# Kernel optimization log

Measured on AMD Instinct MI355X. Metric: run time of the kernel, lower is better.

## Reference

```python
import jax, jax.numpy as jnp
import numpy as np
import math

B, S, E = 2, 2048, 1024
H, HD = 16, 64  # num_heads, head_size


def setup_inputs() -> dict:
    key = jax.random.key(0)
    ks = jax.random.split(key, 9)
    sc = 1.0 / math.sqrt(HD)
    return {
        "x": jax.random.normal(ks[0], (B, S, E), dtype=jnp.float32),
        "Wq_w": jax.random.normal(ks[1], (HD, HD), dtype=jnp.float32) * sc,
        "Wq_b": jax.random.normal(ks[2], (HD,), dtype=jnp.float32) * 0.02,
        "Wk_w": jax.random.normal(ks[3], (HD, HD), dtype=jnp.float32) * sc,
        "Wk_b": jax.random.normal(ks[4], (HD,), dtype=jnp.float32) * 0.02,
        "Wv_w": jax.random.normal(ks[5], (HD, HD), dtype=jnp.float32) * sc,
        "Wv_b": jax.random.normal(ks[6], (HD,), dtype=jnp.float32) * 0.02,
        "proj_w": jax.random.normal(ks[7], (E, E), dtype=jnp.float32) * (1.0 / math.sqrt(E)),
        "proj_b": jax.random.normal(ks[8], (E,), dtype=jnp.float32) * 0.02,
    }


def reference(x, Wq_w, Wq_b, Wk_w, Wk_b, Wv_w, Wv_b, proj_w, proj_b):
    b, s, _ = x.shape
    xh = x.reshape(b, s, H, HD)  # split heads; QKV linears act per-head (shared weights)
    # torch Linear: y = x @ W.T + b
    q = jnp.einsum('bshd,ed->bhse', xh, Wq_w) + Wq_b  # [B,H,S,HD]
    k = jnp.einsum('bshd,ed->bhse', xh, Wk_w) + Wk_b
    v = jnp.einsum('bshd,ed->bhse', xh, Wv_w) + Wv_b
    scores = jnp.einsum('bhqd,bhkd->bhqk', q, k) / math.sqrt(HD)
    causal = jnp.tril(jnp.ones((s, s), dtype=bool))
    scores = jnp.where(causal, scores, jnp.float32(-1e20))
    attn = jax.nn.softmax(scores, axis=-1)  # attn_dropout p=0 (eval)
    out = jnp.einsum('bhqk,bhkd->bqhd', attn, v).reshape(b, s, H * HD)
    out = out @ proj_w.T + proj_b  # resid_dropout p=0 (eval)
    return out
```

## Files before the change

kernel.cpp:

```cpp
#include <hip/hip_runtime.h>
#include <hip/hip_bf16.h>

#define B_ 2
#define S_ 2048
#define E_ 1024
#define H_ 16
#define HD_ 64
#define T_ (B_ * S_)

typedef short bf16x8 __attribute__((ext_vector_type(8)));
typedef short bf16x4 __attribute__((ext_vector_type(4)));
typedef float f32x4 __attribute__((ext_vector_type(4)));

__device__ __forceinline__ short f2bf(float f) {
  union { float f; unsigned u; } v;
  v.f = f;
  unsigned r = v.u + 0x7fffu + ((v.u >> 16) & 1u);
  return (short)(r >> 16);
}

__device__ __forceinline__ int vperm_key(int cc) {
  return (cc & ~31) | (((cc >> 2) & 1) << 4) | (((cc >> 3) & 3) << 2) | (cc & 3);
}

__global__ __launch_bounds__(256) void qkv_conv_kernel(
    const float* __restrict__ x,
    const float* __restrict__ wq, const float* __restrict__ bq,
    const float* __restrict__ wk, const float* __restrict__ bk,
    const float* __restrict__ wv, const float* __restrict__ bv,
    short* __restrict__ Q, short* __restrict__ K, short* __restrict__ V,
    const float* __restrict__ pw, short* __restrict__ pwb) {
  const int tid = threadIdx.x;
  if (blockIdx.x >= 512) {
    int i = ((blockIdx.x - 512) * 256 + tid) * 4;
    float4 f = *(const float4*)(pw + i);
    bf16x4 o;
    o[0] = f2bf(f.x); o[1] = f2bf(f.y); o[2] = f2bf(f.z); o[3] = f2bf(f.w);
    *(bf16x4*)(pwb + i) = o;
    return;
  }
  __shared__ short Xs[64][136];
  __shared__ short Ws[192][72];
  __shared__ short Qt[64][68], Kt[64][68], Vt[64][68];

  const int bid = blockIdx.x;
  const int tb = bid >> 3, hg = bid & 7;
  const int s0 = (tb * 64) & (S_ - 1);
  const int bb = (tb * 64) >> 11;
  const int wave = tid >> 6, lane = tid & 63;
  const int lrow = lane & 15, quad = lane >> 4;

#pragma unroll
  for (int i = 0; i < 8; i++) {
    int c = tid + 256 * i;
    int row = c >> 5, col4 = c & 31;
    float4 f = *(const float4*)(x + ((long)(tb * 64 + row)) * E_ + hg * 128 + col4 * 4);
    bf16x4 o;
    o[0] = f2bf(f.x); o[1] = f2bf(f.y); o[2] = f2bf(f.z); o[3] = f2bf(f.w);
    *(bf16x4*)&Xs[row][col4 * 4] = o;
  }
#pragma unroll
  for (int m = 0; m < 3; m++) {
    const float* w = (m == 0) ? wq : (m == 1) ? wk : wv;
#pragma unroll
    for (int i = 0; i < 4; i++) {
      int c = tid + 256 * i;
      int row = m * 64 + (c >> 4), col = (c & 15) * 4;
      float4 f = *(const float4*)(w + (long)c * 4);
      bf16x4 o;
      o[0] = f2bf(f.x); o[1] = f2bf(f.y); o[2] = f2bf(f.z); o[3] = f2bf(f.w);
      *(bf16x4*)&Ws[row][col] = o;
    }
  }
  float bias[12];
#pragma unroll
  for (int nb = 0; nb < 12; nb++) {
    int sel = nb >> 2;
    int e = ((nb & 3) * 16) + lrow;
    bias[nb] = ((sel == 0) ? bq : (sel == 1) ? bk : bv)[e];
  }
  __syncthreads();

  bf16x8 bf0[12], bf1[12];
#pragma unroll
  for (int nb = 0; nb < 12; nb++) {
    bf0[nb] = *(bf16x8*)&Ws[nb * 16 + lrow][quad * 8];
    bf1[nb] = *(bf16x8*)&Ws[nb * 16 + lrow][32 + quad * 8];
  }

  const float QSCALE = 0.125f * 1.44269504089f;
  for (int hl = 0; hl < 2; hl++) {
    const int h = hg * 2 + hl;
    bf16x8 a0 = *(bf16x8*)&Xs[wave * 16 + lrow][hl * 64 + quad * 8];
    bf16x8 a1 = *(bf16x8*)&Xs[wave * 16 + lrow][hl * 64 + 32 + quad * 8];
#pragma unroll
    for (int nb = 0; nb < 12; nb++) {
      f32x4 acc = {0.f, 0.f, 0.f, 0.f};
      acc = __builtin_amdgcn_mfma_f32_16x16x32_bf16(a0, bf0[nb], acc, 0, 0, 0);
      acc = __builtin_amdgcn_mfma_f32_16x16x32_bf16(a1, bf1[nb], acc, 0, 0, 0);
      const int sel = nb >> 2;
      const float scale = (sel == 0) ? QSCALE : 1.0f;
      short (*ct)[68] = (sel == 0) ? Qt : (sel == 1) ? Kt : Vt;
#pragma unroll
      for (int r = 0; r < 4; r++) {
        ct[wave * 16 + quad * 4 + r][(nb & 3) * 16 + lrow] =
            f2bf((acc[r] + bias[nb]) * scale);
      }
    }
    __syncthreads();

    const int bh = bb * H_ + h;
    short* Qg = Q + ((long)bh * S_ + s0) * HD_;
    short* Kg = K + ((long)bh * S_ + s0) * HD_;
    short* Vg = V + (long)bh * HD_ * S_;
#pragma unroll
    for (int i = 0; i < 2; i++) {
      int c = tid + 256 * i;
      int row = c >> 3, col = (c & 7) * 8;
      *(bf16x8*)(Qg + (long)row * HD_ + col) = *(bf16x8*)&Qt[row][col];
      *(bf16x8*)(Kg + (long)row * HD_ + col) = *(bf16x8*)&Kt[row][col];
      bf16x8 vv;
#pragma unroll
      for (int j = 0; j < 8; j++) {
        int cc = col + j;
        vv[j] = Vt[vperm_key(cc)][row];
      }
      *(bf16x8*)(Vg + (long)row * S_ + s0 + col) = vv;
    }
    __syncthreads();
  }
}

__global__ __launch_bounds__(256, 4) void attn_kernel(
    const short* __restrict__ Q, const short* __restrict__ K,
    const short* __restrict__ Vt, short* __restrict__ O ) {
  __shared__ __align__(16) char RAW[2 * 64 * 72 * 2 * 2];
  short (*Ks)[64][72] = (short (*)[64][72])RAW;
  short (*Vs)[64][72] = (short (*)[64][72])(RAW + 2 * 64 * 72 * 2);
  float (*Cb)[64][20] = (float (*)[64][20])RAW;

  const int tid = threadIdx.x;
  const int bid = blockIdx.x;
  const int bh = bid & 31;
  const int pr = bid >> 5;
  const int b = bh >> 4, h = bh & 15;
  const long base = ((long)bh) << 17;

  const int wave = tid >> 6, lane = tid & 63;
  const int c = wave >> 1;
  const int s = wave & 1;
  const int lrow = lane & 15, quad = lane >> 4;

  const int ct = tid & 127;
  const int r0 = ct >> 1, chc = (ct & 1) * 32;
  const short* Kg = K + base + (long)r0 * HD_ + chc;
  const short* Vg = Vt + base + (long)r0 * S_ + chc;

  bf16x8 kreg[4], vreg[4];
  auto LD = [&](int k0) {
#pragma unroll
    for (int j = 0; j < 4; j++) {
      kreg[j] = *(const bf16x8*)(Kg + (long)k0 * HD_ + 8 * j);
      vreg[j] = *(const bf16x8*)(Vg + k0 + 8 * j);
    }
  };

  const int qts[2] = {pr, 63 - pr};
  LD(c * 64);
  bool nextld = false;

  for (int ph = 0; ph < 2; ph++) {
    const int qt = qts[ph];
    const int nkt = (qt >> 1) + 1;
    const int nc = (nkt + 1 - c) >> 1;
    const int nit = (nkt + 1) >> 1;
    if (ph == 1 && !nextld) LD(c * 64);

    const int qg = qt * 32 + s * 16 + lrow;
    const short* qp = Q + base + (long)qg * HD_;
    bf16x8 qf0 = *(const bf16x8*)(qp + quad * 8);
    bf16x8 qf1 = *(const bf16x8*)(qp + 32 + quad * 8);

    f32x4 Oacc[4];
#pragma unroll
    for (int db = 0; db < 4; db++) Oacc[db] = f32x4{0.f, 0.f, 0.f, 0.f};
    float lsum = 0.f;

    for (int i = 0; i < nit; i++) {
      const bool act = i < nc;
      const int kt = 2 * i + c;
      if (act) {
#pragma unroll
        for (int j = 0; j < 4; j++) {
          *(bf16x8*)&Ks[c][r0][chc + 8 * j] = kreg[j];
          *(bf16x8*)&Vs[c][r0][chc + 8 * j] = vreg[j];
        }
      }
      __syncthreads();
      if (i + 1 < nc) {
        LD((2 * (i + 1) + c) * 64);
      } else if (ph == 0 && i + 1 == nc) {
        LD(c * 64);
        nextld = true;
      }

      if (act) {
        f32x4 sc[4];
#pragma unroll
        for (int nb = 0; nb < 4; nb++) {
          bf16x8 ka0 = *(bf16x8*)&Ks[c][nb * 16 + lrow][quad * 8];
          bf16x8 ka1 = *(bf16x8*)&Ks[c][nb * 16 + lrow][32 + quad * 8];
          f32x4 acc = {0.f, 0.f, 0.f, 0.f};
          acc = __builtin_amdgcn_mfma_f32_16x16x32_bf16(ka0, qf0, acc, 0, 0, 0);
          acc = __builtin_amdgcn_mfma_f32_16x16x32_bf16(ka1, qf1, acc, 0, 0, 0);
          sc[nb] = acc;
        }

        if (kt == nkt - 1) {
          const int k0 = kt * 64;
#pragma unroll
          for (int nb = 0; nb < 4; nb++) {
            int kgl = k0 + nb * 16 + quad * 4;
#pragma unroll
            for (int r = 0; r < 4; r++)
              if (kgl + r > qg) sc[nb][r] = -1e30f;
          }
        }

        bf16x4 pf[4];
#pragma unroll
        for (int nb = 0; nb < 4; nb++) {
          unsigned u[4];
#pragma unroll
          for (int r = 0; r < 4; r++) {
            float p = __builtin_amdgcn_exp2f(sc[nb][r]);
            lsum += p;
            u[r] = __float_as_uint(p) + 0x8000u;
          }
          unsigned lo = __builtin_amdgcn_perm(u[1], u[0], 0x07060302u);
          unsigned hi = __builtin_amdgcn_perm(u[3], u[2], 0x07060302u);
          union { unsigned q[2]; bf16x4 v; } pk;
          pk.q[0] = lo; pk.q[1] = hi;
          pf[nb] = pk.v;
        }

#pragma unroll
        for (int p2 = 0; p2 < 2; p2++) {
#pragma unroll
          for (int db = 0; db < 4; db++) {
            bf16x8 vv = *(bf16x8*)&Vs[c][db * 16 + lrow][p2 * 32 + quad * 8];
            bf16x4 vlo = {vv[0], vv[1], vv[2], vv[3]};
            bf16x4 vhi = {vv[4], vv[5], vv[6], vv[7]};
            Oacc[db] = __builtin_amdgcn_mfma_f32_16x16x16bf16_1k(vlo, pf[2 * p2], Oacc[db], 0, 0, 0);
            Oacc[db] = __builtin_amdgcn_mfma_f32_16x16x16bf16_1k(vhi, pf[2 * p2 + 1], Oacc[db], 0, 0, 0);
          }
        }
      }
      __syncthreads();
    }

    if (c == 1) {
#pragma unroll
      for (int db = 0; db < 4; db++) {
        float4 o4 = make_float4(Oacc[db][0], Oacc[db][1], Oacc[db][2], Oacc[db][3]);
        *(float4*)&Cb[s][lane][db * 4] = o4;
      }
      Cb[s][lane][16] = lsum;
    }
    __syncthreads();
    if (c == 0) {
#pragma unroll
      for (int db = 0; db < 4; db++) {
        float4 o4 = *(float4*)&Cb[s][lane][db * 4];
        Oacc[db][0] += o4.x; Oacc[db][1] += o4.y;
        Oacc[db][2] += o4.z; Oacc[db][3] += o4.w;
      }
      lsum += Cb[s][lane][16];
      lsum += __shfl_xor(lsum, 16);
      lsum += __shfl_xor(lsum, 32);
      const float invl = 1.f / lsum;
      const long token = (long)b * S_ + qg;
      short* obase = O + token * E_ + h * HD_;
#pragma unroll
      for (int db = 0; db < 4; db++) {
        bf16x4 o;
#pragma unroll
        for (int r = 0; r < 4; r++) o[r] = f2bf(Oacc[db][r] * invl);
        *(bf16x4*)(obase + db * 16 + quad * 4) = o;
      }
    }
    __syncthreads();
  }
}

__global__ __launch_bounds__(256) void proj_kernel(
    const short* __restrict__ A, const short* __restrict__ W,
    const float* __restrict__ bias, float* __restrict__ out) {
  __shared__ short As[2][128][40];
  __shared__ short Bs[2][64][40];
  const int tid = threadIdx.x;
  const int bid = blockIdx.x;
  const int m0 = (bid >> 4) * 128;
  const int n0 = (bid & 15) * 64;
  const int wave = tid >> 6, lane = tid & 63;
  const int wm = wave >> 1, wn = wave & 1;
  const int lrow = lane & 15, quad = lane >> 4;

  const int ar = tid >> 1, ac = (tid & 1) * 16;
  const int br = tid >> 2, bc = (tid & 3) * 8;

  bf16x8 a0, a1, b0;
  auto LDR = [&](int k0) {
    const short* ap = A + (long)(m0 + ar) * E_ + k0 + ac;
    a0 = *(const bf16x8*)(ap);
    a1 = *(const bf16x8*)(ap + 8);
    b0 = *(const bf16x8*)(W + (long)(n0 + br) * E_ + k0 + bc);
  };

  f32x4 acc[4][2];
#pragma unroll
  for (int i = 0; i < 4; i++)
#pragma unroll
    for (int j = 0; j < 2; j++) acc[i][j] = f32x4{0.f, 0.f, 0.f, 0.f};

  LDR(0);
  for (int kk = 0; kk < 32; kk++) {
    const int buf = kk & 1;
    *(bf16x8*)&As[buf][ar][ac] = a0;
    *(bf16x8*)&As[buf][ar][ac + 8] = a1;
    *(bf16x8*)&Bs[buf][br][bc] = b0;
    __syncthreads();
    if (kk < 31) LDR((kk + 1) * 32);

    bf16x8 af[4], bfr[2];
#pragma unroll
    for (int i = 0; i < 4; i++)
      af[i] = *(bf16x8*)&As[buf][wm * 64 + i * 16 + lrow][quad * 8];
#pragma unroll
    for (int j = 0; j < 2; j++)
      bfr[j] = *(bf16x8*)&Bs[buf][wn * 32 + j * 16 + lrow][quad * 8];
#pragma unroll
    for (int i = 0; i < 4; i++)
#pragma unroll
      for (int j = 0; j < 2; j++)
        acc[i][j] = __builtin_amdgcn_mfma_f32_16x16x32_bf16(af[i], bfr[j], acc[i][j], 0, 0, 0);
  }

#pragma unroll
  for (int j = 0; j < 2; j++) {
    int col = n0 + wn * 32 + j * 16 + lrow;
    float bv = bias[col];
#pragma unroll
    for (int i = 0; i < 4; i++) {
#pragma unroll
      for (int r = 0; r < 4; r++) {
        int row = m0 + wm * 64 + i * 16 + quad * 4 + r;
        out[(long)row * E_ + col] = acc[i][j][r] + bv;
      }
    }
  }
}

extern "C" void kernel_launch(void* const* d_in, const int* in_sizes, int n_in,
                              void* d_out, int out_size, void* d_ws, size_t ws_size,
                              hipStream_t stream) {
  const float* x  = (const float*)d_in[0];
  const float* wq = (const float*)d_in[1];
  const float* bq = (const float*)d_in[2];
  const float* wk = (const float*)d_in[3];
  const float* bk = (const float*)d_in[4];
  const float* wv = (const float*)d_in[5];
  const float* bv = (const float*)d_in[6];
  const float* pw = (const float*)d_in[7];
  const float* pb = (const float*)d_in[8];
  float* out = (float*)d_out;

  char* ws = (char*)d_ws;
  const size_t qkv_bytes = (size_t)B_ * H_ * S_ * HD_ * 2;
  short* Qb = (short*)(ws);
  short* Kb = (short*)(ws + qkv_bytes);
  short* Vb = (short*)(ws + 2 * qkv_bytes);
  short* AO = (short*)(ws + 3 * qkv_bytes);
  short* PW = (short*)(ws + 3 * qkv_bytes + (size_t)T_ * E_ * 2);

  qkv_conv_kernel<<<dim3(512 + 1024), dim3(256), 0, stream>>>(
      x, wq, bq, wk, bk, wv, bv, Qb, Kb, Vb, pw, PW);
  attn_kernel<<<dim3(32 * 32), dim3(256), 0, stream>>>(Qb, Kb, Vb, AO);
  proj_kernel<<<dim3(32 * 16), dim3(256), 0, stream>>>(AO, PW, pb, out);
}
```

Baseline: 157.8 us.

## Pre-swizzle K/V tiles into MFMA fragment order and restructure attention blocking

```diff
diff --git a/kernel.cpp b/kernel.cpp
--- a/kernel.cpp
+++ b/kernel.cpp
@@ -19,16 +19,13 @@
   return (short)(r >> 16);
 }
 
-__device__ __forceinline__ int vperm_key(int cc) {
-  return (cc & ~31) | (((cc >> 2) & 1) << 4) | (((cc >> 3) & 3) << 2) | (cc & 3);
-}
 
 __global__ __launch_bounds__(256) void qkv_conv_kernel(
     const float* __restrict__ x,
     const float* __restrict__ wq, const float* __restrict__ bq,
     const float* __restrict__ wk, const float* __restrict__ bk,
     const float* __restrict__ wv, const float* __restrict__ bv,
-    short* __restrict__ Q, short* __restrict__ K, short* __restrict__ V,
+    short* __restrict__ Q, short* __restrict__ KV,
     const float* __restrict__ pw, short* __restrict__ pwb) {
   const int tid = threadIdx.x;
   if (blockIdx.x >= 512) {
@@ -46,6 +43,7 @@
   const int bid = blockIdx.x;
   const int tb = bid >> 3, hg = bid & 7;
   const int s0 = (tb * 64) & (S_ - 1);
+  const int kt = s0 >> 6;
   const int bb = (tb * 64) >> 11;
   const int wave = tid >> 6, lane = tid & 63;
   const int lrow = lane & 15, quad = lane >> 4;
@@ -111,73 +109,70 @@
 
     const int bh = bb * H_ + h;
     short* Qg = Q + ((long)bh * S_ + s0) * HD_;
-    short* Kg = K + ((long)bh * S_ + s0) * HD_;
-    short* Vg = V + (long)bh * HD_ * S_;
+    short* Tg = KV + ((long)(bh * 32 + kt)) * 8192;
 #pragma unroll
     for (int i = 0; i < 2; i++) {
       int c = tid + 256 * i;
       int row = c >> 3, col = (c & 7) * 8;
       *(bf16x8*)(Qg + (long)row * HD_ + col) = *(bf16x8*)&Qt[row][col];
-      *(bf16x8*)(Kg + (long)row * HD_ + col) = *(bf16x8*)&Kt[row][col];
-      bf16x8 vv;
-#pragma unroll
-      for (int j = 0; j < 8; j++) {
-        int cc = col + j;
-        vv[j] = Vt[vperm_key(cc)][row];
-      }
-      *(bf16x8*)(Vg + (long)row * S_ + s0 + col) = vv;
+    }
+#pragma unroll
+    for (int u = 0; u < 4; u++) {
+      int fid = tid + 256 * u;
+      bf16x8 val;
+      int lane2 = fid & 63;
+      int quad2 = lane2 >> 4, lrow2 = lane2 & 15;
+      if (u < 2) {
+        int g = fid >> 6;
+        int nb = g >> 1, half = g & 1;
+        val = *(bf16x8*)&Kt[nb * 16 + lrow2][half * 32 + quad2 * 8];
+      } else {
+        int g = (fid >> 6) & 7;
+        int p2 = g >> 2, db = g & 3;
+#pragma unroll
+        for (int j = 0; j < 8; j++) {
+          int key = (2 * p2 + (j >> 2)) * 16 + quad2 * 4 + (j & 3);
+          val[j] = Vt[key][db * 16 + lrow2];
+        }
+      }
+      *(bf16x8*)(Tg + fid * 8) = val;
     }
     __syncthreads();
   }
 }
 
-__global__ __launch_bounds__(256, 4) void attn_kernel(
-    const short* __restrict__ Q, const short* __restrict__ K,
-    const short* __restrict__ Vt, short* __restrict__ O ) {
-  __shared__ __align__(16) char RAW[2 * 64 * 72 * 2 * 2];
-  short (*Ks)[64][72] = (short (*)[64][72])RAW;
-  short (*Vs)[64][72] = (short (*)[64][72])(RAW + 2 * 64 * 72 * 2);
-  float (*Cb)[64][20] = (float (*)[64][20])RAW;
+__global__ __launch_bounds__(256) void attn_kernel(
+    const short* __restrict__ Q, const short* __restrict__ KV,
+    short* __restrict__ O ) {
+  __shared__ short L[2][8192];
 
   const int tid = threadIdx.x;
   const int bid = blockIdx.x;
   const int bh = bid & 31;
   const int pr = bid >> 5;
   const int b = bh >> 4, h = bh & 15;
-  const long base = ((long)bh) << 17;
+  const long qbase = ((long)bh) << 17;
 
   const int wave = tid >> 6, lane = tid & 63;
-  const int c = wave >> 1;
-  const int s = wave & 1;
   const int lrow = lane & 15, quad = lane >> 4;
 
-  const int ct = tid & 127;
-  const int r0 = ct >> 1, chc = (ct & 1) * 32;
-  const short* Kg = K + base + (long)r0 * HD_ + chc;
-  const short* Vg = Vt + base + (long)r0 * S_ + chc;
-
-  bf16x8 kreg[4], vreg[4];
-  auto LD = [&](int k0) {
-#pragma unroll
-    for (int j = 0; j < 4; j++) {
-      kreg[j] = *(const bf16x8*)(Kg + (long)k0 * HD_ + 8 * j);
-      vreg[j] = *(const bf16x8*)(Vg + k0 + 8 * j);
-    }
+  const short* Tg = KV + ((long)bh * 32) * 8192 + tid * 8;
+
+  bf16x8 reg[4];
+  auto LD = [&](int kt) {
+    const short* p = Tg + (long)kt * 8192;
+#pragma unroll
+    for (int u = 0; u < 4; u++) reg[u] = *(const bf16x8*)(p + u * 2048);
   };
 
-  const int qts[2] = {pr, 63 - pr};
-  LD(c * 64);
-  bool nextld = false;
-
+  const int qts[2] = {pr, 31 - pr};
+  LD(0);
+  int it = 0;
   for (int ph = 0; ph < 2; ph++) {
     const int qt = qts[ph];
-    const int nkt = (qt >> 1) + 1;
-    const int nc = (nkt + 1 - c) >> 1;
-    const int nit = (nkt + 1) >> 1;
-    if (ph == 1 && !nextld) LD(c * 64);
-
-    const int qg = qt * 32 + s * 16 + lrow;
-    const short* qp = Q + base + (long)qg * HD_;
+    const int q0w = qt * 64 + wave * 16;
+    const int qg = q0w + lrow;
+    const short* qp = Q + qbase + (long)qg * HD_;
     bf16x8 qf0 = *(const bf16x8*)(qp + quad * 8);
     bf16x8 qf1 = *(const bf16x8*)(qp + 32 + quad * 8);
 
@@ -186,110 +181,87 @@
     for (int db = 0; db < 4; db++) Oacc[db] = f32x4{0.f, 0.f, 0.f, 0.f};
     float lsum = 0.f;
 
-    for (int i = 0; i < nit; i++) {
-      const bool act = i < nc;
-      const int kt = 2 * i + c;
-      if (act) {
-#pragma unroll
-        for (int j = 0; j < 4; j++) {
-          *(bf16x8*)&Ks[c][r0][chc + 8 * j] = kreg[j];
-          *(bf16x8*)&Vs[c][r0][chc + 8 * j] = vreg[j];
-        }
-      }
+    const int nkt = qt + 1;
+    for (int kt = 0; kt < nkt; kt++, it++) {
+      const int buf = it & 1;
+#pragma unroll
+      for (int u = 0; u < 4; u++)
+        *(bf16x8*)&L[buf][(tid + 256 * u) * 8] = reg[u];
       __syncthreads();
-      if (i + 1 < nc) {
-        LD((2 * (i + 1) + c) * 64);
-      } else if (ph == 0 && i + 1 == nc) {
-        LD(c * 64);
-        nextld = true;
-      }
-
-      if (act) {
-        f32x4 sc[4];
+
+      {
+        int ktn = kt + 1;
+        bool have = true;
+        if (ktn == nkt) {
+          if (ph == 0) ktn = 0; else have = false;
+        }
+        if (have) LD(ktn);
+      }
+
+      f32x4 sc[4];
+#pragma unroll
+      for (int nb = 0; nb < 4; nb++) {
+        bf16x8 ka0 = *(bf16x8*)&L[buf][(nb * 2 + 0) * 512 + lane * 8];
+        bf16x8 ka1 = *(bf16x8*)&L[buf][(nb * 2 + 1) * 512 + lane * 8];
+        f32x4 acc = {0.f, 0.f, 0.f, 0.f};
+        acc = __builtin_amdgcn_mfma_f32_16x16x32_bf16(ka0, qf0, acc, 0, 0, 0);
+        acc = __builtin_amdgcn_mfma_f32_16x16x32_bf16(ka1, qf1, acc, 0, 0, 0);
+        sc[nb] = acc;
+      }
+
+      if (kt == qt) {
+        const int k0 = kt * 64;
 #pragma unroll
         for (int nb = 0; nb < 4; nb++) {
-          bf16x8 ka0 = *(bf16x8*)&Ks[c][nb * 16 + lrow][quad * 8];
-          bf16x8 ka1 = *(bf16x8*)&Ks[c][nb * 16 + lrow][32 + quad * 8];
-          f32x4 acc = {0.f, 0.f, 0.f, 0.f};
-          acc = __builtin_amdgcn_mfma_f32_16x16x32_bf16(ka0, qf0, acc, 0, 0, 0);
-          acc = __builtin_amdgcn_mfma_f32_16x16x32_bf16(ka1, qf1, acc, 0, 0, 0);
-          sc[nb] = acc;
-        }
-
-        if (kt == nkt - 1) {
-          const int k0 = kt * 64;
-#pragma unroll
-          for (int nb = 0; nb < 4; nb++) {
-            int kgl = k0 + nb * 16 + quad * 4;
-#pragma unroll
-            for (int r = 0; r < 4; r++)
-              if (kgl + r > qg) sc[nb][r] = -1e30f;
-          }
-        }
-
-        bf16x4 pf[4];
-#pragma unroll
-        for (int nb = 0; nb < 4; nb++) {
-          unsigned u[4];
-#pragma unroll
-          for (int r = 0; r < 4; r++) {
-            float p = __builtin_amdgcn_exp2f(sc[nb][r]);
-            lsum += p;
-            u[r] = __float_as_uint(p) + 0x8000u;
-          }
-          unsigned lo = __builtin_amdgcn_perm(u[1], u[0], 0x07060302u);
-          unsigned hi = __builtin_amdgcn_perm(u[3], u[2], 0x07060302u);
-          union { unsigned q[2]; bf16x4 v; } pk;
-          pk.q[0] = lo; pk.q[1] = hi;
-          pf[nb] = pk.v;
-        }
-
-#pragma unroll
-        for (int p2 = 0; p2 < 2; p2++) {
-#pragma unroll
-          for (int db = 0; db < 4; db++) {
-            bf16x8 vv = *(bf16x8*)&Vs[c][db * 16 + lrow][p2 * 32 + quad * 8];
-            bf16x4 vlo = {vv[0], vv[1], vv[2], vv[3]};
-            bf16x4 vhi = {vv[4], vv[5], vv[6], vv[7]};
-            Oacc[db] = __builtin_amdgcn_mfma_f32_16x16x16bf16_1k(vlo, pf[2 * p2], Oacc[db], 0, 0, 0);
-            Oacc[db] = __builtin_amdgcn_mfma_f32_16x16x16bf16_1k(vhi, pf[2 * p2 + 1], Oacc[db], 0, 0, 0);
-          }
-        }
-      }
-      __syncthreads();
-    }
-
-    if (c == 1) {
-#pragma unroll
-      for (int db = 0; db < 4; db++) {
-        float4 o4 = make_float4(Oacc[db][0], Oacc[db][1], Oacc[db][2], Oacc[db][3]);
-        *(float4*)&Cb[s][lane][db * 4] = o4;
-      }
-      Cb[s][lane][16] = lsum;
-    }
-    __syncthreads();
-    if (c == 0) {
-#pragma unroll
-      for (int db = 0; db < 4; db++) {
-        float4 o4 = *(float4*)&Cb[s][lane][db * 4];
-        Oacc[db][0] += o4.x; Oacc[db][1] += o4.y;
-        Oacc[db][2] += o4.z; Oacc[db][3] += o4.w;
-      }
-      lsum += Cb[s][lane][16];
-      lsum += __shfl_xor(lsum, 16);
-      lsum += __shfl_xor(lsum, 32);
-      const float invl = 1.f / lsum;
-      const long token = (long)b * S_ + qg;
-      short* obase = O + token * E_ + h * HD_;
-#pragma unroll
-      for (int db = 0; db < 4; db++) {
-        bf16x4 o;
-#pragma unroll
-        for (int r = 0; r < 4; r++) o[r] = f2bf(Oacc[db][r] * invl);
-        *(bf16x4*)(obase + db * 16 + quad * 4) = o;
-      }
-    }
-    __syncthreads();
+          int kgl = k0 + nb * 16 + quad * 4;
+#pragma unroll
+          for (int r = 0; r < 4; r++)
+            if (kgl + r > qg) sc[nb][r] = -1e30f;
+        }
+      }
+
+      bf16x4 pf[4];
+#pragma unroll
+      for (int nb = 0; nb < 4; nb++) {
+        unsigned u[4];
+#pragma unroll
+        for (int r = 0; r < 4; r++) {
+          float p = __builtin_amdgcn_exp2f(sc[nb][r]);
+          lsum += p;
+          u[r] = __float_as_uint(p) + 0x8000u;
+        }
+        unsigned lo = __builtin_amdgcn_perm(u[1], u[0], 0x07060302u);
+        unsigned hi = __builtin_amdgcn_perm(u[3], u[2], 0x07060302u);
+        union { unsigned q[2]; bf16x4 v; } pk;
+        pk.q[0] = lo; pk.q[1] = hi;
+        pf[nb] = pk.v;
+      }
+
+#pragma unroll
+      for (int p2 = 0; p2 < 2; p2++) {
+#pragma unroll
+        for (int db = 0; db < 4; db++) {
+          bf16x8 vv = *(bf16x8*)&L[buf][4096 + (p2 * 4 + db) * 512 + lane * 8];
+          bf16x4 vlo = {vv[0], vv[1], vv[2], vv[3]};
+          bf16x4 vhi = {vv[4], vv[5], vv[6], vv[7]};
+          Oacc[db] = __builtin_amdgcn_mfma_f32_16x16x16bf16_1k(vlo, pf[2 * p2], Oacc[db], 0, 0, 0);
+          Oacc[db] = __builtin_amdgcn_mfma_f32_16x16x16bf16_1k(vhi, pf[2 * p2 + 1], Oacc[db], 0, 0, 0);
+        }
+      }
+    }
+
+    lsum += __shfl_xor(lsum, 16);
+    lsum += __shfl_xor(lsum, 32);
+    const float invl = 1.f / lsum;
+    const long token = (long)b * S_ + qg;
+    short* obase = O + token * E_ + h * HD_;
+#pragma unroll
+    for (int db = 0; db < 4; db++) {
+      bf16x4 o;
+#pragma unroll
+      for (int r = 0; r < 4; r++) o[r] = f2bf(Oacc[db][r] * invl);
+      *(bf16x4*)(obase + db * 16 + quad * 4) = o;
+    }
   }
 }
 
@@ -376,15 +348,13 @@
   float* out = (float*)d_out;
 
   char* ws = (char*)d_ws;
-  const size_t qkv_bytes = (size_t)B_ * H_ * S_ * HD_ * 2;
   short* Qb = (short*)(ws);
-  short* Kb = (short*)(ws + qkv_bytes);
-  short* Vb = (short*)(ws + 2 * qkv_bytes);
-  short* AO = (short*)(ws + 3 * qkv_bytes);
-  short* PW = (short*)(ws + 3 * qkv_bytes + (size_t)T_ * E_ * 2);
+  short* KVb = (short*)(ws + (size_t)8 * 1024 * 1024);
+  short* AO = (short*)(ws + (size_t)24 * 1024 * 1024);
+  short* PW = (short*)(ws + (size_t)32 * 1024 * 1024);
 
   qkv_conv_kernel<<<dim3(512 + 1024), dim3(256), 0, stream>>>(
-      x, wq, bq, wk, bk, wv, bv, Qb, Kb, Vb, pw, PW);
-  attn_kernel<<<dim3(32 * 32), dim3(256), 0, stream>>>(Qb, Kb, Vb, AO);
+      x, wq, bq, wk, bk, wv, bv, Qb, KVb, pw, PW);
+  attn_kernel<<<dim3(16 * 32), dim3(256), 0, stream>>>(Qb, KVb, AO);
   proj_kernel<<<dim3(32 * 16), dim3(256), 0, stream>>>(AO, PW, pb, out);
 }
```

Result: faster. 146.6 us (-7.1%).
